# Optimization experiments

Hardware: AMD Instinct MI355X
Metric: run time of the kernel (lower is better)

## Reference

```python
import jax, jax.numpy as jnp
import numpy as np
import math

B, T, L, C = 4, 8, 512, 768
H = 8
HD = C // H  # 96
EPS = 1e-12  # F.normalize eps


def _l2norm(x):
    # F.normalize(x, dim=-1): x / max(||x||2, eps)
    n = jnp.sqrt(jnp.sum(x * x, axis=-1, keepdims=True))
    return x / jnp.maximum(n, EPS)


def setup_inputs() -> dict:
    key = jax.random.key(0)
    ks = jax.random.split(key, 7)
    s = 1.0 / math.sqrt(C)
    x = jax.random.normal(ks[0], (B, T, L, C), dtype=jnp.float32)
    Wq = jax.random.uniform(ks[1], (C, C), jnp.float32, -s, s)
    bq = jax.random.uniform(ks[2], (C,), jnp.float32, -s, s)
    Wkv = jax.random.uniform(ks[3], (C, 2 * C), jnp.float32, -s, s)
    bkv = jax.random.uniform(ks[4], (2 * C,), jnp.float32, -s, s)
    Wm = jax.random.uniform(ks[5], (C, C), jnp.float32, -s, s)
    bm = jax.random.uniform(ks[6], (C,), jnp.float32, -s, s)
    return {"x": x, "Wq": Wq, "bq": bq, "Wkv": Wkv, "bkv": bkv, "Wm": Wm, "bm": bm}


def reference(x, Wq, bq, Wkv, bkv, Wm, bm):
    b, t, l, c = x.shape
    # q: (b,t,l,c) -> (b,t,H,l,hd), L2-normalized over hd
    q = (x @ Wq + bq).reshape(b, t, l, H, HD).transpose(0, 1, 3, 2, 4)
    q = _l2norm(q)
    # kv: (b,t,l,2c) -> (b,t,2H,l,hd); chunk on head axis -> k = heads [0,H), v = heads [H,2H)
    kv = (x @ Wkv + bkv).reshape(b, t, l, 2 * H, HD).transpose(0, 1, 3, 2, 4)
    k = _l2norm(kv[:, :, :H])
    v = _l2norm(kv[:, :, H:])
    # attention (dropout on scores is identity in eval mode)
    scores = jnp.einsum("bthqd,bthkd->bthqk", q, k) / math.sqrt(HD)
    attn = jax.nn.softmax(scores, axis=-1)
    out = jnp.einsum("bthqk,bthkd->bthqd", attn, v)
    # (b,t,H,l,hd) -> (b,t,l,c), output projection (drop2 identity in eval)
    out = out.transpose(0, 1, 3, 2, 4).reshape(b, t, l, c)
    return out @ Wm + bm
```

## Files before the change

kernel.cpp:

```cpp
#include <hip/hip_runtime.h>
#include <hip/hip_bf16.h>


typedef __attribute__((ext_vector_type(8))) short bf16x8;
typedef __attribute__((ext_vector_type(4))) float f32x4;
typedef __attribute__((ext_vector_type(4))) int int4v;

__device__ __forceinline__ float b2f(unsigned short u) {
    return __uint_as_float(((unsigned)u) << 16);
}
__device__ __forceinline__ unsigned short f2b(float f) {
    unsigned u = __float_as_uint(f);
    u = (u + 0x7fffu + ((u >> 16) & 1u)) >> 16;
    return (unsigned short)u;
}

__device__ __forceinline__ void gll16(const unsigned short* g, unsigned short* l) {
    __builtin_amdgcn_global_load_lds((const __attribute__((address_space(1))) unsigned int*)g,
                                     (__attribute__((address_space(3))) unsigned int*)l, 16, 0, 0);
}

#define VMCNT(n) asm volatile("s_waitcnt vmcnt(" #n ")" ::: "memory")
#define BAR()    __builtin_amdgcn_s_barrier()
#define SCHED0() __builtin_amdgcn_sched_barrier(0)
#define PRIO(x)  __builtin_amdgcn_s_setprio(x)

__global__ __launch_bounds__(256) void cast_bf16_k(const float* __restrict__ x,
                                                   unsigned short* __restrict__ xb, int n4) {
    int i = blockIdx.x * 256 + threadIdx.x;
    if (i >= n4) return;
    float4 v = ((const float4*)x)[i];
    ushort4 o;
    o.x = f2b(v.x); o.y = f2b(v.y); o.z = f2b(v.z); o.w = f2b(v.w);
    ((ushort4*)xb)[i] = o;
}

__global__ __launch_bounds__(256) void pack_w_k(const float* __restrict__ Wq,
                                                const float* __restrict__ Wkv,
                                                const float* __restrict__ Wm,
                                                unsigned short* __restrict__ Wt) {
    __shared__ float tile[64][65];
    const int tid = threadIdx.x;
    const int tn = blockIdx.x % 48;
    const int tk = blockIdx.x / 48;
    const int n0 = tn * 64, k0 = tk * 64;
    const float* src; int ldn, coff;
    if (n0 < 768)       { src = Wq;  ldn = 768;  coff = n0; }
    else if (n0 < 2304) { src = Wkv; ldn = 1536; coff = n0 - 768; }
    else                { src = Wm;  ldn = 768;  coff = n0 - 2304; }
    const int j = tid & 63;
    for (int i = tid >> 6; i < 64; i += 4)
        tile[i][j] = src[(k0 + i) * ldn + coff + j];
    __syncthreads();
    const int ii = tid & 63;
    for (int jj = tid >> 6; jj < 64; jj += 4)
        Wt[(long)(n0 + jj) * 768 + k0 + ii] = f2b(tile[ii][jj]);
}

template <int EPI>
__global__ __launch_bounds__(512, 4) void gemm_k(const unsigned short* __restrict__ A,
                                                 const unsigned short* __restrict__ Bt,
                                                 const float* __restrict__ bias0,
                                                 const float* __restrict__ bias1,
                                                 unsigned short* __restrict__ Cb,
                                                 float* __restrict__ Cf,
                                                 int N, int K, int nbn) {
    extern __shared__ unsigned short lds[];
    const int tid = threadIdx.x;
    const int lane = tid & 63, wid = tid >> 6;
    const int wm = wid >> 1, wn = wid & 1;
    const int l15 = lane & 15, g = lane >> 4;

    const int nwg = gridDim.x;
    const int wg = (blockIdx.x & 7) * (nwg >> 3) + (blockIdx.x >> 3);
    const int bm = wg / nbn, bn = wg % nbn;

    const unsigned short* gA = A  + (long)bm * 256 * K;
    const unsigned short* gB = Bt + (long)bn * 128 * K;

    const long sgoff = (long)(tid >> 2) * K + (long)(((tid & 3) ^ ((tid >> 3) & 3)) * 8);
    const int swoff = wid * 512;

#define STAGE_ALL(T, BUFO) do { \
        const long kb0 = (long)(T) * 32; \
        gll16(gB + sgoff + kb0, lds + (BUFO) + 8192 + swoff); \
        gll16(gA + sgoff + kb0, lds + (BUFO) + swoff); \
        gll16(gA + sgoff + kb0 + (long)128 * K, lds + (BUFO) + 4096 + swoff); \
    } while (0)

    const int slot8 = (g ^ ((l15 >> 1) & 3)) * 8;
    f32x4 acc[4][4] = {};
    const int nkt = K >> 5;

    STAGE_ALL(0, 0);
    STAGE_ALL(1, 12288);

    int cur = 0, nx1 = 12288, nx2 = 24576;
    for (int t = 0; t < nkt; ++t) {
        if (t < nkt - 1) { VMCNT(3); } else { VMCNT(0); }
        BAR(); SCHED0();
        if (t + 2 < nkt) STAGE_ALL(t + 2, nx2);

        bf16x8 af[4], bv[4];
#pragma unroll
        for (int mf = 0; mf < 4; mf++)
            af[mf] = *(const bf16x8*)&lds[cur + (wm * 64 + mf * 16 + l15) * 32 + slot8];
#pragma unroll
        for (int nf = 0; nf < 4; nf++)
            bv[nf] = *(const bf16x8*)&lds[cur + 8192 + (wn * 64 + nf * 16 + l15) * 32 + slot8];
        PRIO(1);
#pragma unroll
        for (int mf = 0; mf < 4; mf++)
#pragma unroll
            for (int nf = 0; nf < 4; nf++)
                acc[mf][nf] = __builtin_amdgcn_mfma_f32_16x16x32_bf16(af[mf], bv[nf], acc[mf][nf], 0, 0, 0);
        PRIO(0);
        const int tmp = cur; cur = nx1; nx1 = nx2; nx2 = tmp;
    }
#undef STAGE_ALL

    float bvv[4];
#pragma unroll
    for (int nf = 0; nf < 4; nf++) {
        const int col = bn * 128 + wn * 64 + nf * 16 + l15;
        bvv[nf] = (EPI == 0) ? ((col < 768) ? bias0[col] : bias1[col - 768]) : bias0[col];
    }
#pragma unroll
    for (int mf = 0; mf < 4; mf++) {
#pragma unroll
        for (int r = 0; r < 4; r++) {
            const long row = bm * 256 + wm * 64 + mf * 16 + g * 4 + r;
#pragma unroll
            for (int nf = 0; nf < 4; nf++) {
                const float v = acc[mf][nf][r] + bvv[nf];
                if (EPI == 0) {
                    const unsigned hh = f2b(v);
                    const unsigned oo = __shfl_xor((int)hh, 1);
                    if (!(lane & 1))
                        *(unsigned*)&Cb[row * N + bn * 128 + wn * 64 + nf * 16 + l15] =
                            (hh & 0xffffu) | (oo << 16);
                } else {
                    Cf[row * N + bn * 128 + wn * 64 + nf * 16 + l15] = v;
                }
            }
        }
    }
}

__global__ __launch_bounds__(512, 6) void gemm128_k(const unsigned short* __restrict__ A,
                                                    const unsigned short* __restrict__ Bt,
                                                    const float* __restrict__ bias0,
                                                    float* __restrict__ Cf,
                                                    int N, int K, int nbn) {
    extern __shared__ unsigned short lds[];
    const int tid = threadIdx.x;
    const int lane = tid & 63, wid = tid >> 6;
    const int wm = wid >> 2, wn = wid & 3;
    const int l15 = lane & 15, g = lane >> 4;

    const int nwg = gridDim.x;
    const int wg = (blockIdx.x & 7) * (nwg >> 3) + (blockIdx.x >> 3);
    const int bm = wg / nbn, bn = wg % nbn;

    const unsigned short* gA = A  + (long)bm * 128 * K;
    const unsigned short* gB = Bt + (long)bn * 128 * K;

    const long sgoff = (long)(tid >> 2) * K + (long)(((tid & 3) ^ ((tid >> 3) & 3)) * 8);
    const int swoff = wid * 512;

#define STAGE2(T, BUFO) do { \
        const long kb0 = (long)(T) * 32; \
        gll16(gB + sgoff + kb0, lds + (BUFO) + 4096 + swoff); \
        gll16(gA + sgoff + kb0, lds + (BUFO) + swoff); \
    } while (0)

    const int slot8 = (g ^ ((l15 >> 1) & 3)) * 8;
    f32x4 acc[4][2] = {};
    const int nkt = K >> 5;

    STAGE2(0, 0);
    STAGE2(1, 8192);

    int cur = 0, nx1 = 8192, nx2 = 16384;
    for (int t = 0; t < nkt; ++t) {
        if (t < nkt - 1) { VMCNT(2); } else { VMCNT(0); }
        BAR(); SCHED0();
        if (t + 2 < nkt) STAGE2(t + 2, nx2);

        bf16x8 af[4], bv[2];
#pragma unroll
        for (int mf = 0; mf < 4; mf++)
            af[mf] = *(const bf16x8*)&lds[cur + (wm * 64 + mf * 16 + l15) * 32 + slot8];
#pragma unroll
        for (int nf = 0; nf < 2; nf++)
            bv[nf] = *(const bf16x8*)&lds[cur + 4096 + (wn * 32 + nf * 16 + l15) * 32 + slot8];
        PRIO(1);
#pragma unroll
        for (int mf = 0; mf < 4; mf++)
#pragma unroll
            for (int nf = 0; nf < 2; nf++)
                acc[mf][nf] = __builtin_amdgcn_mfma_f32_16x16x32_bf16(af[mf], bv[nf], acc[mf][nf], 0, 0, 0);
        PRIO(0);
        const int tmp = cur; cur = nx1; nx1 = nx2; nx2 = tmp;
    }
#undef STAGE2

    float bvv[2];
#pragma unroll
    for (int nf = 0; nf < 2; nf++)
        bvv[nf] = bias0[bn * 128 + wn * 32 + nf * 16 + l15];
#pragma unroll
    for (int mf = 0; mf < 4; mf++) {
#pragma unroll
        for (int r = 0; r < 4; r++) {
            const long row = bm * 128 + wm * 64 + mf * 16 + g * 4 + r;
#pragma unroll
            for (int nf = 0; nf < 2; nf++)
                Cf[row * N + bn * 128 + wn * 32 + nf * 16 + l15] = acc[mf][nf][r] + bvv[nf];
        }
    }
}

__global__ __launch_bounds__(256) void knvn_k(const unsigned short* __restrict__ qkv,
                                              float* __restrict__ kinv,
                                              float* __restrict__ vinv) {
    const int tid = threadIdx.x, lane = tid & 63, w = tid >> 6;
    const int s = blockIdx.x * 4 + w;
    const int row = s >> 3, h = s & 7;
    const unsigned short* pk = qkv + (long)row * 2304 + 768 + h * 96;
    float k0 = 0.f, k1 = 0.f, v0 = 0.f, v1 = 0.f;
    if (lane < 48) {
        unsigned a = *(const unsigned*)(pk + lane * 2);
        unsigned b = *(const unsigned*)(pk + 768 + lane * 2);
        k0 = b2f((unsigned short)(a & 0xffffu)); k1 = b2f((unsigned short)(a >> 16));
        v0 = b2f((unsigned short)(b & 0xffffu)); v1 = b2f((unsigned short)(b >> 16));
    }
    float sk = k0 * k0 + k1 * k1;
    float sv = v0 * v0 + v1 * v1;
#pragma unroll
    for (int m = 1; m < 64; m <<= 1) { sk += __shfl_xor(sk, m); sv += __shfl_xor(sv, m); }
    if (lane == 0) {
        kinv[h * 16384 + row] = 1.f / fmaxf(sqrtf(sk), 1e-12f);
        vinv[h * 16384 + row] = 1.f / fmaxf(sqrtf(sv), 1e-12f);
    }
}

__global__ __launch_bounds__(256, 4) void attn_k(const unsigned short* __restrict__ qkv,
                                                 const float* __restrict__ kinv,
                                                 const float* __restrict__ vinv,
                                                 unsigned short* __restrict__ obuf) {
    constexpr float SCALE = 0.1020620726159658f;
    __shared__ unsigned short Ps[64 * 72];
    __shared__ unsigned short Ks[64 * 104];
    __shared__ unsigned short Vt[96 * 72];
    __shared__ float kinv_s[64], vinv_s[64];

    const int tid = threadIdx.x, lane = tid & 63, w = tid >> 6;
    const int bid0 = blockIdx.x;
    const int bid = (bid0 & 7) * 256 + (bid0 >> 3);
    const int qt = bid & 7, h = (bid >> 3) & 7, bt = bid >> 6;
    const long rowbase = (long)bt * 512 * 2304 + h * 96;
    const int l15 = lane & 15;
    const int g = lane >> 4;
    const int ko = g * 8;

    bf16x8 qf[3];
    {
        const unsigned short* qrow = qkv + rowbase + (long)(qt * 64 + w * 16 + l15) * 2304;
#pragma unroll
        for (int ks = 0; ks < 3; ks++)
            qf[ks] = *(const bf16x8*)&qrow[ks * 32 + ko];
    }
    for (int j = 0; j < 3; j++) {
        const int c = tid + j * 256;
        const int r = c / 12, d8 = (c % 12) * 8;
        *(int4v*)&Ks[r * 104 + d8] = *(const int4v*)&qkv[rowbase + 768 + (long)r * 2304 + d8];
    }
    for (int j = 0; j < 3; j++) {
        const int c = tid + j * 256;
        const int key = c & 63, d8 = (c >> 6) * 8;
        int4v vv = *(const int4v*)&qkv[rowbase + 1536 + (long)key * 2304 + d8];
        const unsigned short* vp = (const unsigned short*)&vv;
#pragma unroll
        for (int i = 0; i < 8; i++) Vt[(d8 + i) * 72 + key] = vp[i];
    }
    if (tid < 64)       kinv_s[tid]      = kinv[h * 16384 + bt * 512 + tid];
    else if (tid < 128) vinv_s[tid - 64] = vinv[h * 16384 + bt * 512 + tid - 64];
    __syncthreads();

    float ssq = 0.f;
#pragma unroll
    for (int ks = 0; ks < 3; ks++)
#pragma unroll
        for (int j = 0; j < 8; j++) {
            const float f = b2f((unsigned short)qf[ks][j]);
            ssq += f * f;
        }
    ssq += __shfl_xor(ssq, 16);
    ssq += __shfl_xor(ssq, 32);
    const float qs = SCALE / fmaxf(sqrtf(ssq), 1e-12f);

    float l_run = 0.f;
    f32x4 oacc[6] = {};

    for (int kt = 0; kt < 8; kt++) {
        f32x4 sacc[4] = {};
#pragma unroll
        for (int ks = 0; ks < 3; ks++) {
#pragma unroll
            for (int kf = 0; kf < 4; kf++) {
                bf16x8 af = *(const bf16x8*)&Ks[(kf * 16 + l15) * 104 + ks * 32 + ko];
                sacc[kf] = __builtin_amdgcn_mfma_f32_16x16x32_bf16(af, qf[ks], sacc[kf], 0, 0, 0);
            }
        }

        float p[16];
        float s = 0.f;
#pragma unroll
        for (int kf = 0; kf < 4; kf++)
#pragma unroll
            for (int r = 0; r < 4; r++) {
                const float pv = __expf(sacc[kf][r] * qs * kinv_s[kf * 16 + g * 4 + r]);
                s += pv;
                p[kf * 4 + r] = pv * vinv_s[kf * 16 + g * 4 + r];
            }
        s += __shfl_xor(s, 16);
        s += __shfl_xor(s, 32);
        l_run += s;

        {
            unsigned* prow = (unsigned*)&Ps[(w * 16 + l15) * 72];
#pragma unroll
            for (int kf = 0; kf < 4; kf++)
#pragma unroll
                for (int rp = 0; rp < 2; rp++) {
                    unsigned pk = (unsigned)f2b(p[kf * 4 + 2 * rp]) |
                                  ((unsigned)f2b(p[kf * 4 + 2 * rp + 1]) << 16);
                    prow[kf * 8 + g * 2 + rp] = pk;
                }
        }

#pragma unroll
        for (int ks = 0; ks < 2; ks++) {
            bf16x8 pa = *(const bf16x8*)&Ps[(w * 16 + l15) * 72 + ks * 32 + ko];
#pragma unroll
            for (int nf = 0; nf < 6; nf++) {
                bf16x8 vb = *(const bf16x8*)&Vt[(nf * 16 + l15) * 72 + ks * 32 + ko];
                oacc[nf] = __builtin_amdgcn_mfma_f32_16x16x32_bf16(pa, vb, oacc[nf], 0, 0, 0);
            }
        }
        __syncthreads();

        if (kt < 7) {
            const int kn = kt + 1;
            for (int j = 0; j < 3; j++) {
                const int c = tid + j * 256;
                const int r = c / 12, d8 = (c % 12) * 8;
                *(int4v*)&Ks[r * 104 + d8] =
                    *(const int4v*)&qkv[rowbase + 768 + (long)(kn * 64 + r) * 2304 + d8];
            }
            for (int j = 0; j < 3; j++) {
                const int c = tid + j * 256;
                const int key = c & 63, d8 = (c >> 6) * 8;
                int4v vv = *(const int4v*)&qkv[rowbase + 1536 + (long)(kn * 64 + key) * 2304 + d8];
                const unsigned short* vp = (const unsigned short*)&vv;
#pragma unroll
                for (int i = 0; i < 8; i++) Vt[(d8 + i) * 72 + key] = vp[i];
            }
            if (tid < 64)       kinv_s[tid]      = kinv[h * 16384 + bt * 512 + kn * 64 + tid];
            else if (tid < 128) vinv_s[tid - 64] = vinv[h * 16384 + bt * 512 + kn * 64 + tid - 64];
            __syncthreads();
        }
    }

    const float inv = 1.f / l_run;
    float invr[4];
#pragma unroll
    for (int r = 0; r < 4; r++) invr[r] = __shfl(inv, g * 4 + r);
#pragma unroll
    for (int r = 0; r < 4; r++) {
        const int row = w * 16 + g * 4 + r;
        const long gr = ((long)(bt * 512 + qt * 64 + row)) * 768 + h * 96;
#pragma unroll
        for (int nf = 0; nf < 6; nf++)
            obuf[gr + nf * 16 + l15] = f2b(oacc[nf][r] * invr[r]);
    }
}

extern "C" void kernel_launch(void* const* d_in, const int* in_sizes, int n_in,
                              void* d_out, int out_size, void* d_ws, size_t ws_size,
                              hipStream_t stream) {
    const float* x   = (const float*)d_in[0];
    const float* Wq  = (const float*)d_in[1];
    const float* bq  = (const float*)d_in[2];
    const float* Wkv = (const float*)d_in[3];
    const float* bkv = (const float*)d_in[4];
    const float* Wm  = (const float*)d_in[5];
    const float* bm  = (const float*)d_in[6];
    float* out = (float*)d_out;

    char* ws = (char*)d_ws;
    unsigned short* xb  = (unsigned short*)ws;
    float*          vinv = (float*)ws;
    float*          kinv = (float*)(ws + 524288);
    unsigned short* wt  = (unsigned short*)(ws + 25165824);
    unsigned short* qkv = (unsigned short*)(ws + 29884416);
    unsigned short* ob  = (unsigned short*)(ws + 105381888);

    static bool attr_set = false;
    if (!attr_set) {
        hipFuncSetAttribute((const void*)gemm_k<0>, hipFuncAttributeMaxDynamicSharedMemorySize, 73728);
        hipFuncSetAttribute((const void*)gemm128_k, hipFuncAttributeMaxDynamicSharedMemorySize, 49152);
        attr_set = true;
    }

    cast_bf16_k<<<dim3(12288), dim3(256), 0, stream>>>(x, xb, 3145728);
    pack_w_k<<<dim3(576), dim3(256), 0, stream>>>(Wq, Wkv, Wm, wt);
    gemm_k<0><<<dim3(1152), dim3(512), 73728, stream>>>(xb, wt, bq, bkv, qkv, nullptr, 2304, 768, 18);
    knvn_k<<<dim3(32768), dim3(256), 0, stream>>>(qkv, kinv, vinv);
    attn_k<<<dim3(2048), dim3(256), 0, stream>>>(qkv, kinv, vinv, ob);
    gemm128_k<<<dim3(768), dim3(512), 49152, stream>>>(ob, wt + (long)2304 * 768, bm, out, 768, 768, 6);
}
```

Baseline: 204.8 us.

## Double-buffer GEMM with less LDS; enlarge attention tile and prefetch K/V into registers

The QKV GEMM drops from a triple-buffered to a double-buffered LDS pipeline with an extra barrier, cutting dynamic LDS from 73728 to 49152 bytes and raising the launch-bound occupancy hint from 4 to 6. The attention kernel now runs 512 threads on 128 query rows per block, which halves how often each K/V tile is reloaded. It stages Q through LDS, reuses that buffer for P, and prefetches the next K/V tile into registers while computing the current one. V is transposed as packed 32-bit pairs instead of 16-bit scatters. The trade-off is a shallower GEMM prefetch and more register pressure in attention.

```diff
diff --git a/kernel.cpp b/kernel.cpp
--- a/kernel.cpp
+++ b/kernel.cpp
@@ -58,7 +58,7 @@
 }
 
 template <int EPI>
-__global__ __launch_bounds__(512, 4) void gemm_k(const unsigned short* __restrict__ A,
+__global__ __launch_bounds__(512, 6) void gemm_k(const unsigned short* __restrict__ A,
                                                  const unsigned short* __restrict__ Bt,
                                                  const float* __restrict__ bias0,
                                                  const float* __restrict__ bias1,
@@ -93,13 +93,12 @@
     const int nkt = K >> 5;
 
     STAGE_ALL(0, 0);
-    STAGE_ALL(1, 12288);
-
-    int cur = 0, nx1 = 12288, nx2 = 24576;
+
+    int cur = 0, nxt = 12288;
     for (int t = 0; t < nkt; ++t) {
+        if (t + 1 < nkt) STAGE_ALL(t + 1, nxt);
         if (t < nkt - 1) { VMCNT(3); } else { VMCNT(0); }
         BAR(); SCHED0();
-        if (t + 2 < nkt) STAGE_ALL(t + 2, nx2);
 
         bf16x8 af[4], bv[4];
 #pragma unroll
@@ -115,7 +114,8 @@
             for (int nf = 0; nf < 4; nf++)
                 acc[mf][nf] = __builtin_amdgcn_mfma_f32_16x16x32_bf16(af[mf], bv[nf], acc[mf][nf], 0, 0, 0);
         PRIO(0);
-        const int tmp = cur; cur = nx1; nx1 = nx2; nx2 = tmp;
+        BAR();
+        const int tmp = cur; cur = nxt; nxt = tmp;
     }
 #undef STAGE_ALL
 
@@ -245,49 +245,64 @@
     }
 }
 
-__global__ __launch_bounds__(256, 4) void attn_k(const unsigned short* __restrict__ qkv,
+__global__ __launch_bounds__(512, 2) void attn_k(const unsigned short* __restrict__ qkv,
                                                  const float* __restrict__ kinv,
                                                  const float* __restrict__ vinv,
                                                  unsigned short* __restrict__ obuf) {
     constexpr float SCALE = 0.1020620726159658f;
-    __shared__ unsigned short Ps[64 * 72];
+    __shared__ unsigned short Qs[128 * 104];
     __shared__ unsigned short Ks[64 * 104];
     __shared__ unsigned short Vt[96 * 72];
-    __shared__ float kinv_s[64], vinv_s[64];
+    __shared__ float kinv_s[2][64], vinv_s[2][64];
 
     const int tid = threadIdx.x, lane = tid & 63, w = tid >> 6;
     const int bid0 = blockIdx.x;
-    const int bid = (bid0 & 7) * 256 + (bid0 >> 3);
-    const int qt = bid & 7, h = (bid >> 3) & 7, bt = bid >> 6;
+    const int bid = (bid0 & 7) * 128 + (bid0 >> 3);
+    const int qt = bid & 3, h = (bid >> 2) & 7, bt = bid >> 5;
     const long rowbase = (long)bt * 512 * 2304 + h * 96;
     const int l15 = lane & 15;
     const int g = lane >> 4;
     const int ko = g * 8;
 
+    for (int j = 0; j < 3; j++) {
+        const int c = tid + j * 512;
+        const int r = c / 12, d8 = (c % 12) * 8;
+        *(int4v*)&Qs[r * 104 + d8] = *(const int4v*)&qkv[rowbase + (long)(qt * 128 + r) * 2304 + d8];
+    }
+    if (tid < 256) {
+#pragma unroll
+        for (int j = 0; j < 3; j++) {
+            const int c = tid + j * 256;
+            const int r = c / 12, d8 = (c % 12) * 8;
+            *(int4v*)&Ks[r * 104 + d8] = *(const int4v*)&qkv[rowbase + 768 + (long)r * 2304 + d8];
+        }
+    } else {
+        const int tid2 = tid - 256;
+#pragma unroll
+        for (int j = 0; j < 2; j++) {
+            const int c = tid2 + j * 256;
+            if (c < 384) {
+                const int kp = c & 31, d8c = c >> 5;
+                const unsigned short* vsrc = &qkv[rowbase + 1536 + (long)(2 * kp) * 2304 + d8c * 8];
+                int4v v0 = *(const int4v*)vsrc;
+                int4v v1 = *(const int4v*)(vsrc + 2304);
+                const unsigned short* p0 = (const unsigned short*)&v0;
+                const unsigned short* p1 = (const unsigned short*)&v1;
+#pragma unroll
+                for (int i = 0; i < 8; i++)
+                    *(unsigned*)&Vt[(d8c * 8 + i) * 72 + 2 * kp] =
+                        (unsigned)p0[i] | ((unsigned)p1[i] << 16);
+            }
+        }
+    }
+    if (tid < 64)       kinv_s[0][tid]      = kinv[h * 16384 + bt * 512 + tid];
+    else if (tid < 128) vinv_s[0][tid - 64] = vinv[h * 16384 + bt * 512 + tid - 64];
+    __syncthreads();
+
     bf16x8 qf[3];
-    {
-        const unsigned short* qrow = qkv + rowbase + (long)(qt * 64 + w * 16 + l15) * 2304;
-#pragma unroll
-        for (int ks = 0; ks < 3; ks++)
-            qf[ks] = *(const bf16x8*)&qrow[ks * 32 + ko];
-    }
-    for (int j = 0; j < 3; j++) {
-        const int c = tid + j * 256;
-        const int r = c / 12, d8 = (c % 12) * 8;
-        *(int4v*)&Ks[r * 104 + d8] = *(const int4v*)&qkv[rowbase + 768 + (long)r * 2304 + d8];
-    }
-    for (int j = 0; j < 3; j++) {
-        const int c = tid + j * 256;
-        const int key = c & 63, d8 = (c >> 6) * 8;
-        int4v vv = *(const int4v*)&qkv[rowbase + 1536 + (long)key * 2304 + d8];
-        const unsigned short* vp = (const unsigned short*)&vv;
-#pragma unroll
-        for (int i = 0; i < 8; i++) Vt[(d8 + i) * 72 + key] = vp[i];
-    }
-    if (tid < 64)       kinv_s[tid]      = kinv[h * 16384 + bt * 512 + tid];
-    else if (tid < 128) vinv_s[tid - 64] = vinv[h * 16384 + bt * 512 + tid - 64];
-    __syncthreads();
-
+#pragma unroll
+    for (int ks = 0; ks < 3; ks++)
+        qf[ks] = *(const bf16x8*)&Qs[(w * 16 + l15) * 104 + ks * 32 + ko];
     float ssq = 0.f;
 #pragma unroll
     for (int ks = 0; ks < 3; ks++)
@@ -304,6 +319,36 @@
     f32x4 oacc[6] = {};
 
     for (int kt = 0; kt < 8; kt++) {
+        const int cb = kt & 1, nb = cb ^ 1;
+
+        int4v preg[4];
+        float tn = 0.f;
+        if (kt < 7) {
+            if (tid < 256) {
+                const long kb = rowbase + 768 + (long)((kt + 1) * 64) * 2304;
+#pragma unroll
+                for (int j = 0; j < 3; j++) {
+                    const int c = tid + j * 256;
+                    preg[j] = *(const int4v*)&qkv[kb + (long)(c / 12) * 2304 + (c % 12) * 8];
+                }
+            } else {
+                const int tid2 = tid - 256;
+                const long vb = rowbase + 1536 + (long)((kt + 1) * 64) * 2304;
+#pragma unroll
+                for (int j = 0; j < 2; j++) {
+                    const int c = tid2 + j * 256;
+                    if (c < 384) {
+                        const int kp = c & 31, d8c = c >> 5;
+                        const unsigned short* vsrc = &qkv[vb + (long)(2 * kp) * 2304 + d8c * 8];
+                        preg[2 * j]     = *(const int4v*)vsrc;
+                        preg[2 * j + 1] = *(const int4v*)(vsrc + 2304);
+                    }
+                }
+            }
+            if (tid < 64)       tn = kinv[h * 16384 + bt * 512 + (kt + 1) * 64 + tid];
+            else if (tid < 128) tn = vinv[h * 16384 + bt * 512 + (kt + 1) * 64 + tid - 64];
+        }
+
         f32x4 sacc[4] = {};
 #pragma unroll
         for (int ks = 0; ks < 3; ks++) {
@@ -320,16 +365,16 @@
         for (int kf = 0; kf < 4; kf++)
 #pragma unroll
             for (int r = 0; r < 4; r++) {
-                const float pv = __expf(sacc[kf][r] * qs * kinv_s[kf * 16 + g * 4 + r]);
+                const float pv = __expf(sacc[kf][r] * qs * kinv_s[cb][kf * 16 + g * 4 + r]);
                 s += pv;
-                p[kf * 4 + r] = pv * vinv_s[kf * 16 + g * 4 + r];
+                p[kf * 4 + r] = pv * vinv_s[cb][kf * 16 + g * 4 + r];
             }
         s += __shfl_xor(s, 16);
         s += __shfl_xor(s, 32);
         l_run += s;
 
         {
-            unsigned* prow = (unsigned*)&Ps[(w * 16 + l15) * 72];
+            unsigned* prow = (unsigned*)&Qs[(w * 16 + l15) * 104];
 #pragma unroll
             for (int kf = 0; kf < 4; kf++)
 #pragma unroll
@@ -342,7 +387,7 @@
 
 #pragma unroll
         for (int ks = 0; ks < 2; ks++) {
-            bf16x8 pa = *(const bf16x8*)&Ps[(w * 16 + l15) * 72 + ks * 32 + ko];
+            bf16x8 pa = *(const bf16x8*)&Qs[(w * 16 + l15) * 104 + ks * 32 + ko];
 #pragma unroll
             for (int nf = 0; nf < 6; nf++) {
                 bf16x8 vb = *(const bf16x8*)&Vt[(nf * 16 + l15) * 72 + ks * 32 + ko];
@@ -352,23 +397,30 @@
         __syncthreads();
 
         if (kt < 7) {
-            const int kn = kt + 1;
-            for (int j = 0; j < 3; j++) {
-                const int c = tid + j * 256;
-                const int r = c / 12, d8 = (c % 12) * 8;
-                *(int4v*)&Ks[r * 104 + d8] =
-                    *(const int4v*)&qkv[rowbase + 768 + (long)(kn * 64 + r) * 2304 + d8];
-            }
-            for (int j = 0; j < 3; j++) {
-                const int c = tid + j * 256;
-                const int key = c & 63, d8 = (c >> 6) * 8;
-                int4v vv = *(const int4v*)&qkv[rowbase + 1536 + (long)(kn * 64 + key) * 2304 + d8];
-                const unsigned short* vp = (const unsigned short*)&vv;
-#pragma unroll
-                for (int i = 0; i < 8; i++) Vt[(d8 + i) * 72 + key] = vp[i];
-            }
-            if (tid < 64)       kinv_s[tid]      = kinv[h * 16384 + bt * 512 + kn * 64 + tid];
-            else if (tid < 128) vinv_s[tid - 64] = vinv[h * 16384 + bt * 512 + kn * 64 + tid - 64];
+            if (tid < 256) {
+#pragma unroll
+                for (int j = 0; j < 3; j++) {
+                    const int c = tid + j * 256;
+                    *(int4v*)&Ks[(c / 12) * 104 + (c % 12) * 8] = preg[j];
+                }
+            } else {
+                const int tid2 = tid - 256;
+#pragma unroll
+                for (int j = 0; j < 2; j++) {
+                    const int c = tid2 + j * 256;
+                    if (c < 384) {
+                        const int kp = c & 31, d8c = c >> 5;
+                        const unsigned short* p0 = (const unsigned short*)&preg[2 * j];
+                        const unsigned short* p1 = (const unsigned short*)&preg[2 * j + 1];
+#pragma unroll
+                        for (int i = 0; i < 8; i++)
+                            *(unsigned*)&Vt[(d8c * 8 + i) * 72 + 2 * kp] =
+                                (unsigned)p0[i] | ((unsigned)p1[i] << 16);
+                    }
+                }
+            }
+            if (tid < 64)       kinv_s[nb][tid]      = tn;
+            else if (tid < 128) vinv_s[nb][tid - 64] = tn;
             __syncthreads();
         }
     }
@@ -380,7 +432,7 @@
 #pragma unroll
     for (int r = 0; r < 4; r++) {
         const int row = w * 16 + g * 4 + r;
-        const long gr = ((long)(bt * 512 + qt * 64 + row)) * 768 + h * 96;
+        const long gr = ((long)(bt * 512 + qt * 128 + row)) * 768 + h * 96;
 #pragma unroll
         for (int nf = 0; nf < 6; nf++)
             obuf[gr + nf * 16 + l15] = f2b(oacc[nf][r] * invr[r]);
@@ -409,15 +461,15 @@
 
     static bool attr_set = false;
     if (!attr_set) {
-        hipFuncSetAttribute((const void*)gemm_k<0>, hipFuncAttributeMaxDynamicSharedMemorySize, 73728);
+        hipFuncSetAttribute((const void*)gemm_k<0>, hipFuncAttributeMaxDynamicSharedMemorySize, 49152);
         hipFuncSetAttribute((const void*)gemm128_k, hipFuncAttributeMaxDynamicSharedMemorySize, 49152);
         attr_set = true;
     }
 
     cast_bf16_k<<<dim3(12288), dim3(256), 0, stream>>>(x, xb, 3145728);
     pack_w_k<<<dim3(576), dim3(256), 0, stream>>>(Wq, Wkv, Wm, wt);
-    gemm_k<0><<<dim3(1152), dim3(512), 73728, stream>>>(xb, wt, bq, bkv, qkv, nullptr, 2304, 768, 18);
+    gemm_k<0><<<dim3(1152), dim3(512), 49152, stream>>>(xb, wt, bq, bkv, qkv, nullptr, 2304, 768, 18);
     knvn_k<<<dim3(32768), dim3(256), 0, stream>>>(qkv, kinv, vinv);
-    attn_k<<<dim3(2048), dim3(256), 0, stream>>>(qkv, kinv, vinv, ob);
+    attn_k<<<dim3(1024), dim3(512), 0, stream>>>(qkv, kinv, vinv, ob);
     gemm128_k<<<dim3(768), dim3(512), 49152, stream>>>(ob, wt + (long)2304 * 768, bm, out, 768, 768, 6);
 }
```

Result: slower. 634.0 us (+209.6%).

## Double attention query tile to 128 rows per block with split K/V staging

Applied to the files above, without the earlier changes.

Attention blocks now hold 8 waves (512 threads) covering 128 query rows, so each staged K/V tile is shared by twice as many queries and the grid halves. K staging is done by the first 256 threads while the other 256 transpose V, packing two keys per 32-bit LDS write instead of single 16-bit stores. This cuts global K/V traffic and LDS store count per query. The cost is larger blocks with more LDS for P, and a fixed occupancy target of 6 in the launch bounds that may constrain registers.

```diff
diff --git a/kernel.cpp b/kernel.cpp
--- a/kernel.cpp
+++ b/kernel.cpp
@@ -245,20 +245,20 @@
     }
 }
 
-__global__ __launch_bounds__(256, 4) void attn_k(const unsigned short* __restrict__ qkv,
+__global__ __launch_bounds__(512, 6) void attn_k(const unsigned short* __restrict__ qkv,
                                                  const float* __restrict__ kinv,
                                                  const float* __restrict__ vinv,
                                                  unsigned short* __restrict__ obuf) {
     constexpr float SCALE = 0.1020620726159658f;
-    __shared__ unsigned short Ps[64 * 72];
+    __shared__ unsigned short Ps[128 * 72];
     __shared__ unsigned short Ks[64 * 104];
     __shared__ unsigned short Vt[96 * 72];
     __shared__ float kinv_s[64], vinv_s[64];
 
     const int tid = threadIdx.x, lane = tid & 63, w = tid >> 6;
     const int bid0 = blockIdx.x;
-    const int bid = (bid0 & 7) * 256 + (bid0 >> 3);
-    const int qt = bid & 7, h = (bid >> 3) & 7, bt = bid >> 6;
+    const int bid = (bid0 & 7) * 128 + (bid0 >> 3);
+    const int qt = bid & 3, h = (bid >> 2) & 7, bt = bid >> 5;
     const long rowbase = (long)bt * 512 * 2304 + h * 96;
     const int l15 = lane & 15;
     const int g = lane >> 4;
@@ -266,26 +266,45 @@
 
     bf16x8 qf[3];
     {
-        const unsigned short* qrow = qkv + rowbase + (long)(qt * 64 + w * 16 + l15) * 2304;
+        const unsigned short* qrow = qkv + rowbase + (long)(qt * 128 + w * 16 + l15) * 2304;
 #pragma unroll
         for (int ks = 0; ks < 3; ks++)
             qf[ks] = *(const bf16x8*)&qrow[ks * 32 + ko];
     }
-    for (int j = 0; j < 3; j++) {
-        const int c = tid + j * 256;
-        const int r = c / 12, d8 = (c % 12) * 8;
-        *(int4v*)&Ks[r * 104 + d8] = *(const int4v*)&qkv[rowbase + 768 + (long)r * 2304 + d8];
-    }
-    for (int j = 0; j < 3; j++) {
-        const int c = tid + j * 256;
-        const int key = c & 63, d8 = (c >> 6) * 8;
-        int4v vv = *(const int4v*)&qkv[rowbase + 1536 + (long)key * 2304 + d8];
-        const unsigned short* vp = (const unsigned short*)&vv;
-#pragma unroll
-        for (int i = 0; i < 8; i++) Vt[(d8 + i) * 72 + key] = vp[i];
-    }
-    if (tid < 64)       kinv_s[tid]      = kinv[h * 16384 + bt * 512 + tid];
-    else if (tid < 128) vinv_s[tid - 64] = vinv[h * 16384 + bt * 512 + tid - 64];
+
+    auto stageKV = [&](int kt) {
+        if (tid < 256) {
+#pragma unroll
+            for (int j = 0; j < 3; j++) {
+                const int c = tid + j * 256;
+                const int r = c / 12, d8 = (c % 12) * 8;
+                *(int4v*)&Ks[r * 104 + d8] =
+                    *(const int4v*)&qkv[rowbase + 768 + (long)(kt * 64 + r) * 2304 + d8];
+            }
+        } else {
+            const int tid2 = tid - 256;
+#pragma unroll
+            for (int j = 0; j < 2; j++) {
+                const int c = tid2 + j * 256;
+                if (c < 384) {
+                    const int kp = c & 31, d8c = c >> 5;
+                    const unsigned short* vsrc =
+                        &qkv[rowbase + 1536 + (long)(kt * 64 + 2 * kp) * 2304 + d8c * 8];
+                    int4v v0 = *(const int4v*)vsrc;
+                    int4v v1 = *(const int4v*)(vsrc + 2304);
+                    const unsigned short* p0 = (const unsigned short*)&v0;
+                    const unsigned short* p1 = (const unsigned short*)&v1;
+#pragma unroll
+                    for (int i = 0; i < 8; i++)
+                        *(unsigned*)&Vt[(d8c * 8 + i) * 72 + 2 * kp] =
+                            (unsigned)p0[i] | ((unsigned)p1[i] << 16);
+                }
+            }
+        }
+        if (tid < 64)       kinv_s[tid]      = kinv[h * 16384 + bt * 512 + kt * 64 + tid];
+        else if (tid < 128) vinv_s[tid - 64] = vinv[h * 16384 + bt * 512 + kt * 64 + tid - 64];
+    };
+    stageKV(0);
     __syncthreads();
 
     float ssq = 0.f;
@@ -352,23 +371,7 @@
         __syncthreads();
 
         if (kt < 7) {
-            const int kn = kt + 1;
-            for (int j = 0; j < 3; j++) {
-                const int c = tid + j * 256;
-                const int r = c / 12, d8 = (c % 12) * 8;
-                *(int4v*)&Ks[r * 104 + d8] =
-                    *(const int4v*)&qkv[rowbase + 768 + (long)(kn * 64 + r) * 2304 + d8];
-            }
-            for (int j = 0; j < 3; j++) {
-                const int c = tid + j * 256;
-                const int key = c & 63, d8 = (c >> 6) * 8;
-                int4v vv = *(const int4v*)&qkv[rowbase + 1536 + (long)(kn * 64 + key) * 2304 + d8];
-                const unsigned short* vp = (const unsigned short*)&vv;
-#pragma unroll
-                for (int i = 0; i < 8; i++) Vt[(d8 + i) * 72 + key] = vp[i];
-            }
-            if (tid < 64)       kinv_s[tid]      = kinv[h * 16384 + bt * 512 + kn * 64 + tid];
-            else if (tid < 128) vinv_s[tid - 64] = vinv[h * 16384 + bt * 512 + kn * 64 + tid - 64];
+            stageKV(kt + 1);
             __syncthreads();
         }
     }
@@ -380,7 +383,7 @@
 #pragma unroll
     for (int r = 0; r < 4; r++) {
         const int row = w * 16 + g * 4 + r;
-        const long gr = ((long)(bt * 512 + qt * 64 + row)) * 768 + h * 96;
+        const long gr = ((long)(bt * 512 + qt * 128 + row)) * 768 + h * 96;
 #pragma unroll
         for (int nf = 0; nf < 6; nf++)
             obuf[gr + nf * 16 + l15] = f2b(oacc[nf][r] * invr[r]);
@@ -418,6 +421,6 @@
     pack_w_k<<<dim3(576), dim3(256), 0, stream>>>(Wq, Wkv, Wm, wt);
     gemm_k<0><<<dim3(1152), dim3(512), 73728, stream>>>(xb, wt, bq, bkv, qkv, nullptr, 2304, 768, 18);
     knvn_k<<<dim3(32768), dim3(256), 0, stream>>>(qkv, kinv, vinv);
-    attn_k<<<dim3(2048), dim3(256), 0, stream>>>(qkv, kinv, vinv, ob);
+    attn_k<<<dim3(1024), dim3(512), 0, stream>>>(qkv, kinv, vinv, ob);
     gemm128_k<<<dim3(768), dim3(512), 49152, stream>>>(ob, wt + (long)2304 * 768, bm, out, 768, 768, 6);
 }
```

Result: slower. 217.5 us (+6.2%).
